# Optimization experiments

Hardware: AMD Instinct MI355X
Metric: run time of the kernel (lower is better)

## Reference

```python
import jax, jax.numpy as jnp
import numpy as np

MAX_DEPTH = 7
FEAT = 32
HIDDEN = 64
RES = 2 ** MAX_DEPTH          # 128
N_VOXELS = RES ** 3           # 2^21 = 2,097,152
BATCH = 4_194_304


def setup_inputs() -> dict:
    key = jax.random.key(0)
    k = jax.random.split(key, 5)
    positions = jax.random.uniform(k[0], (BATCH, 3), dtype=jnp.float32)  # in [0,1)
    # learned parameters (torch: randn table; Linear default-init approximated)
    table = jax.random.normal(k[1], (N_VOXELS, FEAT), dtype=jnp.float32)
    W1 = jax.random.normal(k[2], (FEAT, HIDDEN), dtype=jnp.float32) * (1.0 / np.sqrt(FEAT))
    b1 = jnp.zeros((HIDDEN,), dtype=jnp.float32)
    W2 = jax.random.normal(k[3], (HIDDEN, 4), dtype=jnp.float32) * (1.0 / np.sqrt(HIDDEN))
    b2 = jnp.zeros((4,), dtype=jnp.float32)
    return {"positions": positions, "table": table, "W1": W1, "b1": b1, "W2": W2, "b2": b2}


def reference(positions, table, W1, b1, W2, b2):
    # voxel index per axis; positions in [0,1) so trunc == floor (matches .long())
    idx = jnp.clip((positions * RES).astype(jnp.int32), 0, RES - 1)  # [B,3]
    flat = idx[..., 0] * (RES * RES) + idx[..., 1] * RES + idx[..., 2]  # [B]
    feats = table[flat]                               # irregular gather [B,FEAT]
    h = jax.nn.relu(feats @ W1 + b1)                  # [B,64]
    out = h @ W2 + b2                                 # [B,4]
    rgb = jax.nn.sigmoid(out[..., :3])                # [B,3]
    density = jax.nn.softplus(out[..., 3:4])          # [B,1]
    return rgb, density
```

## Files before the change

kernel.cpp:

```cpp
#include <hip/hip_runtime.h>
#include <hip/hip_bf16.h>

typedef __attribute__((ext_vector_type(8))) short bs8;
typedef __attribute__((ext_vector_type(4))) short bs4;
typedef __attribute__((ext_vector_type(4))) float f32x4;

#define HID 64
#define FEATN 32
#define NT 16

static __device__ __forceinline__ short f2bf(float f) {
    __hip_bfloat16 h = __float2bfloat16(f);
    return __builtin_bit_cast(short, h);
}

#if defined(__HIP_DEVICE_COMPILE__)
#define MFMA16(a, b, c) __builtin_amdgcn_mfma_f32_16x16x16bf16_1k(a, b, c, 0, 0, 0)
#else
#define MFMA16(a, b, c) (c)
#endif

__global__ __launch_bounds__(256, 4) void plen_fused(
    const float* __restrict__ pos,
    const float* __restrict__ table,
    const float* __restrict__ W1,
    const float* __restrict__ b1,
    const float* __restrict__ W2,
    const float* __restrict__ b2,
    float* __restrict__ out,
    int batch)
{
    const int lane = threadIdx.x & 63;
    const int row  = lane & 15;
    const int g    = lane >> 4;

    bs8   w1f[4];
    f32x4 bias1v[4];
    bs4   w2tf[4];
#pragma unroll
    for (int j = 0; j < 4; ++j) {
#pragma unroll
        for (int i = 0; i < 8; ++i)
            w1f[j][i] = f2bf(W1[(g * 8 + i) * HID + j * 16 + row]);
        bias1v[j] = *(const f32x4*)(b1 + j * 16 + g * 4);
#pragma unroll
        for (int i = 0; i < 4; ++i)
            w2tf[j][i] = (row < 4) ? f2bf(W2[(j * 16 + g * 4 + i) * 4 + row]) : (short)0;
    }
    f32x4 oinit;
    if (g == 0) oinit = *(const f32x4*)b2;
    else        oinit = (f32x4){0.f, 0.f, 0.f, 0.f};

    const int wave_id = blockIdx.x * 4 + (threadIdx.x >> 6);
    const int chunk   = wave_id * (NT * 16);
    const size_t dns_base = (size_t)batch * 3;

    auto loadpos = [&](int t, float& x, float& y, float& z) {
        const int tt = t < NT ? t : NT - 1;
        const float* pp = pos + (size_t)(chunk + tt * 16 + row) * 3;
        x = pp[0]; y = pp[1]; z = pp[2];
    };
    auto issue_gather = [&](float x, float y, float z, f32x4& A, f32x4& B) {
        const unsigned ix = (unsigned)(int)(x * 128.0f);
        const unsigned iy = (unsigned)(int)(y * 128.0f);
        const unsigned iz = (unsigned)(int)(z * 128.0f);
        const unsigned flat = (ix << 14) | (iy << 7) | iz;
        const float* rp = table + (size_t)flat * FEATN + g * 8;
        A = *(const f32x4*)rp;
        B = *(const f32x4*)(rp + 4);
    };
    auto compute = [&](int sbase, f32x4 f0, f32x4 f1) {
        bs8 af;
        af[0] = f2bf(f0[0]); af[1] = f2bf(f0[1]);
        af[2] = f2bf(f0[2]); af[3] = f2bf(f0[3]);
        af[4] = f2bf(f1[0]); af[5] = f2bf(f1[1]);
        af[6] = f2bf(f1[2]); af[7] = f2bf(f1[3]);

        f32x4 acc[4];
#pragma unroll
        for (int j = 0; j < 4; ++j)
            acc[j] = __builtin_amdgcn_mfma_f32_16x16x32_bf16(w1f[j], af, bias1v[j], 0, 0, 0);

        f32x4 oacc = oinit;
#pragma unroll
        for (int j = 0; j < 4; ++j) {
            bs4 pf;
            pf[0] = f2bf(fmaxf(acc[j][0], 0.0f));
            pf[1] = f2bf(fmaxf(acc[j][1], 0.0f));
            pf[2] = f2bf(fmaxf(acc[j][2], 0.0f));
            pf[3] = f2bf(fmaxf(acc[j][3], 0.0f));
            oacc = MFMA16(w2tf[j], pf, oacc);
        }

        const float r0 = __builtin_amdgcn_rcpf(1.0f + __expf(-oacc[0]));
        const float r1 = __builtin_amdgcn_rcpf(1.0f + __expf(-oacc[1]));
        const float r2 = __builtin_amdgcn_rcpf(1.0f + __expf(-oacc[2]));
        const float dv = oacc[3];
        const float dn = fmaxf(dv, 0.0f) + __logf(1.0f + __expf(-fabsf(dv)));

        if (g == 0) {
            const int s = sbase + row;
            float* rp = out + (size_t)s * 3;
            __builtin_nontemporal_store(r0, rp);
            __builtin_nontemporal_store(r1, rp + 1);
            __builtin_nontemporal_store(r2, rp + 2);
            __builtin_nontemporal_store(dn, out + dns_base + s);
        }
    };

    float pxA, pyA, pzA, pxB, pyB, pzB;
    f32x4 gA0, gA1, gB0, gB1;
    loadpos(0, pxA, pyA, pzA);
    loadpos(1, pxB, pyB, pzB);
    issue_gather(pxA, pyA, pzA, gA0, gA1);

    for (int t = 0; t < NT; t += 2) {
        loadpos(t + 2, pxA, pyA, pzA);
        issue_gather(pxB, pyB, pzB, gB0, gB1);
        compute(chunk + t * 16, gA0, gA1);

        loadpos(t + 3, pxB, pyB, pzB);
        issue_gather(pxA, pyA, pzA, gA0, gA1);
        compute(chunk + (t + 1) * 16, gB0, gB1);
    }
}

extern "C" void kernel_launch(void* const* d_in, const int* in_sizes, int n_in,
                              void* d_out, int out_size, void* d_ws, size_t ws_size,
                              hipStream_t stream) {
    const float* pos   = (const float*)d_in[0];
    const float* table = (const float*)d_in[1];
    const float* W1    = (const float*)d_in[2];
    const float* b1    = (const float*)d_in[3];
    const float* W2    = (const float*)d_in[4];
    const float* b2    = (const float*)d_in[5];
    float* out = (float*)d_out;

    const int batch  = in_sizes[0] / 3;
    const int blocks = batch / (4 * NT * 16);
    hipLaunchKernelGGL(plen_fused, dim3(blocks), dim3(256), 0, stream,
                       pos, table, W1, b1, W2, b2, out, batch);
}
```

Before: 119.0 us.

## Deepen gather software pipeline from two to four stages

Replaces the two-buffer ping-pong of position loads and table gathers with a four-slot rotating pipeline. Three gathers are kept in flight ahead of compute, and positions are loaded five tiles ahead. The aim is to hide more of the random-access gather latency per wave. In exchange it uses more VGPRs, which at launch bounds (256,4) could force spills or reduce occupancy.

New measurement: 120.2 us. About the same (+1.0%).

```diff
diff --git a/kernel.cpp b/kernel.cpp
--- a/kernel.cpp
+++ b/kernel.cpp
@@ -55,20 +55,6 @@
     const int chunk   = wave_id * (NT * 16);
     const size_t dns_base = (size_t)batch * 3;
 
-    auto loadpos = [&](int t, float& x, float& y, float& z) {
-        const int tt = t < NT ? t : NT - 1;
-        const float* pp = pos + (size_t)(chunk + tt * 16 + row) * 3;
-        x = pp[0]; y = pp[1]; z = pp[2];
-    };
-    auto issue_gather = [&](float x, float y, float z, f32x4& A, f32x4& B) {
-        const unsigned ix = (unsigned)(int)(x * 128.0f);
-        const unsigned iy = (unsigned)(int)(y * 128.0f);
-        const unsigned iz = (unsigned)(int)(z * 128.0f);
-        const unsigned flat = (ix << 14) | (iy << 7) | iz;
-        const float* rp = table + (size_t)flat * FEATN + g * 8;
-        A = *(const f32x4*)rp;
-        B = *(const f32x4*)(rp + 4);
-    };
     auto compute = [&](int sbase, f32x4 f0, f32x4 f1) {
         bs8 af;
         af[0] = f2bf(f0[0]); af[1] = f2bf(f0[1]);
@@ -108,21 +94,44 @@
         }
     };
 
-    float pxA, pyA, pzA, pxB, pyB, pzB;
-    f32x4 gA0, gA1, gB0, gB1;
-    loadpos(0, pxA, pyA, pzA);
-    loadpos(1, pxB, pyB, pzB);
-    issue_gather(pxA, pyA, pzA, gA0, gA1);
+    float Px0, Py0, Pz0, Px1, Py1, Pz1, Px2, Py2, Pz2, Px3, Py3, Pz3;
+    f32x4 Ga0, Gb0, Ga1, Gb1, Ga2, Gb2, Ga3, Gb3;
 
-    for (int t = 0; t < NT; t += 2) {
-        loadpos(t + 2, pxA, pyA, pzA);
-        issue_gather(pxB, pyB, pzB, gB0, gB1);
-        compute(chunk + t * 16, gA0, gA1);
+#define LOADPOS(t, i) do {                                               \
+        const int tt_ = (t) < NT ? (t) : NT - 1;                         \
+        const float* pp_ = pos + (size_t)(chunk + tt_ * 16 + row) * 3;   \
+        Px##i = pp_[0]; Py##i = pp_[1]; Pz##i = pp_[2];                  \
+    } while (0)
 
-        loadpos(t + 3, pxB, pyB, pzB);
-        issue_gather(pxA, pyA, pzA, gA0, gA1);
-        compute(chunk + (t + 1) * 16, gB0, gB1);
+#define GATHER(i) do {                                                   \
+        const unsigned ix_ = (unsigned)(int)(Px##i * 128.0f);            \
+        const unsigned iy_ = (unsigned)(int)(Py##i * 128.0f);            \
+        const unsigned iz_ = (unsigned)(int)(Pz##i * 128.0f);            \
+        const unsigned flat_ = (ix_ << 14) | (iy_ << 7) | iz_;           \
+        const float* rp_ = table + (size_t)flat_ * FEATN + g * 8;        \
+        Ga##i = *(const f32x4*)rp_;                                      \
+        Gb##i = *(const f32x4*)(rp_ + 4);                                \
+    } while (0)
+
+#define STEP(t, gp, lp, cb) do {                                         \
+        GATHER(gp);                                                      \
+        LOADPOS((t) + 5, lp);                                            \
+        compute(chunk + (t) * 16, Ga##cb, Gb##cb);                       \
+    } while (0)
+
+    LOADPOS(0, 0); LOADPOS(1, 1); LOADPOS(2, 2); LOADPOS(3, 3);
+    GATHER(0); GATHER(1); GATHER(2);
+    LOADPOS(4, 0);
+
+    for (int t = 0; t < NT; t += 4) {
+        STEP(t + 0, 3, 1, 0);
+        STEP(t + 1, 0, 2, 1);
+        STEP(t + 2, 1, 3, 2);
+        STEP(t + 3, 2, 0, 3);
     }
+#undef STEP
+#undef GATHER
+#undef LOADPOS
 }
 
 extern "C" void kernel_launch(void* const* d_in, const int* in_sizes, int n_in,
```
